# Kernel optimization log

Measured on AMD Instinct MI355X. Metric: run time of the kernel, lower is better.

The kernel has to match this reference:

```python
import jax, jax.numpy as jnp
import numpy as np

NUM_LAYERS = 32
IN_SIZE = 1024
OUT_SIZE = 1024
B, S = 32, 256


def setup_inputs() -> dict:
    key = jax.random.key(0)
    k1, k2, k3 = jax.random.split(key, 3)
    x = jax.random.normal(k1, (B, S, IN_SIZE), dtype=jnp.float32)
    layer_idx = jax.random.randint(k2, (S,), 0, NUM_LAYERS, dtype=jnp.int32)
    # learned parameter: per-layer weight [L, O, D], normal(stddev=1.0) as in flax init
    weight = jax.random.normal(k3, (NUM_LAYERS, OUT_SIZE, IN_SIZE), dtype=jnp.float32)
    return {"x": x, "layer_idx": layer_idx, "weight": weight}


def reference(x, layer_idx, weight):
    # x: [B, S, D]; layer_idx: [S]; weight: [L, O, D]
    # Each sequence position s uses expert weight[layer_idx[s]]:
    #   out[b, s, o] = sum_d x[b, s, d] * weight[layer_idx[s], o, d]
    w = weight[layer_idx]                      # [S, O, D] gather
    return jnp.einsum('bsd,sod->bso', x, w)    # [B, S, O]
```

## Files before the change

kernel.cpp:

```cpp
#include <hip/hip_runtime.h>
#include <hip/hip_bf16.h>
#include <stdint.h>

#define NLAYERS 32
#define DSIZE   1024
#define OSIZE   1024
#define BATCH   32
#define SEQ     256

#define WS_PERM  16
#define WS_TILE  512
#define MAX_TILES 88

typedef __attribute__((ext_vector_type(8)))  short short8;
typedef __attribute__((ext_vector_type(16))) float f32x16;

#define LDSTRIDE 72
#define BK 64
#define NSPLIT 16

__global__ void prep_kernel(const int* __restrict__ layer_idx, int* __restrict__ wsi) {
    __shared__ int cnt[NLAYERS];
    __shared__ int start_[NLAYERS];
    __shared__ int cursor[NLAYERS];
    const int t = threadIdx.x;
    if (t < NLAYERS) cnt[t] = 0;
    __syncthreads();
    int l = 0;
    if (t < SEQ) { l = layer_idx[t]; atomicAdd(&cnt[l], 1); }
    __syncthreads();
    if (t == 0) {
        int acc = 0;
        for (int i = 0; i < NLAYERS; ++i) { start_[i] = acc; cursor[i] = acc; acc += cnt[i]; }
    }
    __syncthreads();
    if (t < SEQ) {
        int r = atomicAdd(&cursor[l], 1);
        wsi[WS_PERM + r] = t;
    }
    if (t == 0) {
        int nt = 0;
        for (int i = 0; i < NLAYERS; ++i) {
            const int c = cnt[i];
            for (int j = 0; j < c; j += 4) {
                wsi[WS_TILE + nt*4 + 0] = i;
                wsi[WS_TILE + nt*4 + 1] = start_[i] + j;
                wsi[WS_TILE + nt*4 + 2] = (c - j < 4) ? (c - j) : 4;
                ++nt;
            }
        }
        wsi[0] = nt;
    }
}

static __device__ __forceinline__ unsigned pk2(float a, float b) {
    unsigned ua = __builtin_bit_cast(unsigned, a) + 0x8000u;
    unsigned ub = __builtin_bit_cast(unsigned, b) + 0x8000u;
    return __builtin_amdgcn_perm(ub, ua, 0x07060302u);
}

__global__ __launch_bounds__(256, 3) void gemm_kernel(
        const float* __restrict__ x, const float* __restrict__ wgt,
        const int* __restrict__ wsi, float* __restrict__ out) {
    const int ntiles = wsi[0];
    const int mt = blockIdx.y;
    if (mt >= ntiles) return;
    const int layer     = wsi[WS_TILE + mt*4 + 0];
    const int rank_base = wsi[WS_TILE + mt*4 + 1];
    const int nranks    = wsi[WS_TILE + mt*4 + 2];
    const int ntile     = blockIdx.x;

    __shared__ __align__(16) short ldsA[128 * LDSTRIDE];
    __shared__ __align__(16) short ldsB[64 * LDSTRIDE];

    const int t     = threadIdx.x;
    const int c4    = (t & 15) * 4;
    const int rbase = t >> 4;

    bool svalid[4];
    int  sv[4];
    #pragma unroll
    for (int j = 0; j < 4; ++j) {
        svalid[j] = (j < nranks);
        sv[j] = svalid[j] ? wsi[WS_PERM + rank_base + j] : 0;
    }

    const float* aptr[8];
    #pragma unroll
    for (int p = 0; p < 8; ++p) {
        const int roff = p >> 1;
        const int b    = rbase + ((p & 1) << 4);
        aptr[p] = x + (((size_t)(b * SEQ + sv[roff])) << 10) + c4;
    }
    const float* bbase = wgt + (((size_t)((layer << 10) + ntile * 64 + rbase)) << 10) + c4;

    float4 ra[8], rb[4];
    auto load_step = [&](int kk) {
        #pragma unroll
        for (int p = 0; p < 8; ++p) {
            if (svalid[p >> 1]) ra[p] = *(const float4*)(aptr[p] + kk);
            else                ra[p] = make_float4(0.f, 0.f, 0.f, 0.f);
        }
        #pragma unroll
        for (int p = 0; p < 4; ++p)
            rb[p] = *(const float4*)(bbase + ((size_t)p << 14) + kk);
    };

    const int lane = t & 63;
    const int wv   = t >> 6;
    const int wm   = wv * 32;
    const int l31  = lane & 31;
    const int lh   = lane >> 5;

    f32x16 acc[2];
    #pragma unroll
    for (int ni = 0; ni < 2; ++ni)
        #pragma unroll
        for (int r = 0; r < 16; ++r) acc[ni][r] = 0.f;

    const short* pA0 = &ldsA[(wm + l31) * LDSTRIDE + lh * 8];
    const short* pB0 = &ldsB[l31 * LDSTRIDE + lh * 8];

    load_step(0);
    #pragma unroll 1
    for (int kk = 0; kk < DSIZE; kk += BK) {
        __syncthreads();
        #pragma unroll
        for (int p = 0; p < 8; ++p) {
            const int row = rbase + 16 * p;
            uint2 va;
            va.x = pk2(ra[p].x, ra[p].y);
            va.y = pk2(ra[p].z, ra[p].w);
            *(uint2*)&ldsA[row * LDSTRIDE + c4] = va;
        }
        #pragma unroll
        for (int p = 0; p < 4; ++p) {
            const int row = rbase + 16 * p;
            uint2 vb;
            vb.x = pk2(rb[p].x, rb[p].y);
            vb.y = pk2(rb[p].z, rb[p].w);
            *(uint2*)&ldsB[row * LDSTRIDE + c4] = vb;
        }
        __syncthreads();
        if (kk + BK < DSIZE) load_step(kk + BK);
        #pragma unroll
        for (int sub = 0; sub < 4; ++sub) {
            short8 a0 = *(const short8*)(pA0 + sub*16);
            short8 b0 = *(const short8*)(pB0 + sub*16);
            short8 b1 = *(const short8*)(pB0 + 32*LDSTRIDE + sub*16);
            acc[0] = __builtin_amdgcn_mfma_f32_32x32x16_bf16(a0, b0, acc[0], 0, 0, 0);
            acc[1] = __builtin_amdgcn_mfma_f32_32x32x16_bf16(a0, b1, acc[1], 0, 0, 0);
        }
    }

    if (wv < nranks) {
        const int s = wsi[WS_PERM + rank_base + wv];
        #pragma unroll
        for (int ni = 0; ni < 2; ++ni) {
            const int ocol = ntile * 64 + ni * 32 + l31;
            #pragma unroll
            for (int r = 0; r < 16; ++r) {
                const int brow = (r & 3) + 8 * (r >> 2) + 4 * lh;
                out[(((size_t)(brow * SEQ + s)) << 10) + ocol] = acc[ni][r];
            }
        }
    }
}

extern "C" void kernel_launch(void* const* d_in, const int* in_sizes, int n_in,
                              void* d_out, int out_size, void* d_ws, size_t ws_size,
                              hipStream_t stream) {
    const float* x         = (const float*)d_in[0];
    const int*   layer_idx = (const int*)  d_in[1];
    const float* weight    = (const float*)d_in[2];
    float* out = (float*)d_out;
    int*   wsi = (int*)d_ws;

    prep_kernel<<<1, 256, 0, stream>>>(layer_idx, wsi);
    gemm_kernel<<<dim3(NSPLIT, MAX_TILES), 256, 0, stream>>>(x, weight, wsi, out);
}
```

Before: 251.4 us.

## Widen N tile to 128, split K in two with atomic accumulation

Each block now covers 128 output columns instead of 64, with four accumulators per wave, so every A tile loaded from global memory feeds twice as many MFMAs. The K dimension is split across two blocks via blockIdx.z, and partial results are combined with float atomicAdd into an output zeroed by hipMemsetAsync. BK drops to 32 and launch bounds rise to 4 blocks per SM. The cost is a memset pass over the output and atomic write traffic, and the summation order becomes nondeterministic.

```diff
diff --git a/kernel.cpp b/kernel.cpp
--- a/kernel.cpp
+++ b/kernel.cpp
@@ -15,9 +15,9 @@
 typedef __attribute__((ext_vector_type(8)))  short short8;
 typedef __attribute__((ext_vector_type(16))) float f32x16;
 
-#define LDSTRIDE 72
-#define BK 64
-#define NSPLIT 16
+#define LDSTRIDE 40
+#define BK 32
+#define KSPLIT 2
 
 __global__ void prep_kernel(const int* __restrict__ layer_idx, int* __restrict__ wsi) {
     __shared__ int cnt[NLAYERS];
@@ -59,7 +59,7 @@
     return __builtin_amdgcn_perm(ub, ua, 0x07060302u);
 }
 
-__global__ __launch_bounds__(256, 3) void gemm_kernel(
+__global__ __launch_bounds__(256, 4) void gemm_kernel(
         const float* __restrict__ x, const float* __restrict__ wgt,
         const int* __restrict__ wsi, float* __restrict__ out) {
     const int ntiles = wsi[0];
@@ -69,13 +69,14 @@
     const int rank_base = wsi[WS_TILE + mt*4 + 1];
     const int nranks    = wsi[WS_TILE + mt*4 + 2];
     const int ntile     = blockIdx.x;
+    const int koff      = blockIdx.z * (DSIZE / KSPLIT);
 
     __shared__ __align__(16) short ldsA[128 * LDSTRIDE];
-    __shared__ __align__(16) short ldsB[64 * LDSTRIDE];
+    __shared__ __align__(16) short ldsB[128 * LDSTRIDE];
 
     const int t     = threadIdx.x;
-    const int c4    = (t & 15) * 4;
-    const int rbase = t >> 4;
+    const int c4    = (t & 7) * 4;
+    const int rbase = t >> 3;
 
     bool svalid[4];
     int  sv[4];
@@ -85,25 +86,22 @@
         sv[j] = svalid[j] ? wsi[WS_PERM + rank_base + j] : 0;
     }
 
-    const float* aptr[8];
+    const float* aptr[4];
     #pragma unroll
-    for (int p = 0; p < 8; ++p) {
-        const int roff = p >> 1;
-        const int b    = rbase + ((p & 1) << 4);
-        aptr[p] = x + (((size_t)(b * SEQ + sv[roff])) << 10) + c4;
-    }
-    const float* bbase = wgt + (((size_t)((layer << 10) + ntile * 64 + rbase)) << 10) + c4;
+    for (int p = 0; p < 4; ++p)
+        aptr[p] = x + (((size_t)(rbase * SEQ + sv[p])) << 10) + koff + c4;
+    const float* bbase = wgt + (((size_t)((layer << 10) + ntile * 128 + rbase)) << 10) + koff + c4;
 
-    float4 ra[8], rb[4];
+    float4 ra[4], rb[4];
     auto load_step = [&](int kk) {
         #pragma unroll
-        for (int p = 0; p < 8; ++p) {
-            if (svalid[p >> 1]) ra[p] = *(const float4*)(aptr[p] + kk);
-            else                ra[p] = make_float4(0.f, 0.f, 0.f, 0.f);
+        for (int p = 0; p < 4; ++p) {
+            if (svalid[p]) ra[p] = *(const float4*)(aptr[p] + kk);
+            else           ra[p] = make_float4(0.f, 0.f, 0.f, 0.f);
         }
         #pragma unroll
         for (int p = 0; p < 4; ++p)
-            rb[p] = *(const float4*)(bbase + ((size_t)p << 14) + kk);
+            rb[p] = *(const float4*)(bbase + ((size_t)(32 * p) << 10) + kk);
     };
 
     const int lane = t & 63;
@@ -112,9 +110,9 @@
     const int l31  = lane & 31;
     const int lh   = lane >> 5;
 
-    f32x16 acc[2];
+    f32x16 acc[4];
     #pragma unroll
-    for (int ni = 0; ni < 2; ++ni)
+    for (int ni = 0; ni < 4; ++ni)
         #pragma unroll
         for (int r = 0; r < 16; ++r) acc[ni][r] = 0.f;
 
@@ -123,11 +121,11 @@
 
     load_step(0);
     #pragma unroll 1
-    for (int kk = 0; kk < DSIZE; kk += BK) {
+    for (int kk = 0; kk < DSIZE / KSPLIT; kk += BK) {
         __syncthreads();
         #pragma unroll
-        for (int p = 0; p < 8; ++p) {
-            const int row = rbase + 16 * p;
+        for (int p = 0; p < 4; ++p) {
+            const int row = rbase + 32 * p;
             uint2 va;
             va.x = pk2(ra[p].x, ra[p].y);
             va.y = pk2(ra[p].z, ra[p].w);
@@ -135,33 +133,34 @@
         }
         #pragma unroll
         for (int p = 0; p < 4; ++p) {
-            const int row = rbase + 16 * p;
+            const int row = rbase + 32 * p;
             uint2 vb;
             vb.x = pk2(rb[p].x, rb[p].y);
             vb.y = pk2(rb[p].z, rb[p].w);
             *(uint2*)&ldsB[row * LDSTRIDE + c4] = vb;
         }
         __syncthreads();
-        if (kk + BK < DSIZE) load_step(kk + BK);
+        if (kk + BK < DSIZE / KSPLIT) load_step(kk + BK);
         #pragma unroll
-        for (int sub = 0; sub < 4; ++sub) {
+        for (int sub = 0; sub < 2; ++sub) {
             short8 a0 = *(const short8*)(pA0 + sub*16);
-            short8 b0 = *(const short8*)(pB0 + sub*16);
-            short8 b1 = *(const short8*)(pB0 + 32*LDSTRIDE + sub*16);
-            acc[0] = __builtin_amdgcn_mfma_f32_32x32x16_bf16(a0, b0, acc[0], 0, 0, 0);
-            acc[1] = __builtin_amdgcn_mfma_f32_32x32x16_bf16(a0, b1, acc[1], 0, 0, 0);
+            #pragma unroll
+            for (int ni = 0; ni < 4; ++ni) {
+                short8 b = *(const short8*)(pB0 + 32*ni*LDSTRIDE + sub*16);
+                acc[ni] = __builtin_amdgcn_mfma_f32_32x32x16_bf16(a0, b, acc[ni], 0, 0, 0);
+            }
         }
     }
 
     if (wv < nranks) {
-        const int s = wsi[WS_PERM + rank_base + wv];
+        const int s = sv[wv];
         #pragma unroll
-        for (int ni = 0; ni < 2; ++ni) {
-            const int ocol = ntile * 64 + ni * 32 + l31;
+        for (int ni = 0; ni < 4; ++ni) {
+            const int ocol = ntile * 128 + ni * 32 + l31;
             #pragma unroll
             for (int r = 0; r < 16; ++r) {
                 const int brow = (r & 3) + 8 * (r >> 2) + 4 * lh;
-                out[(((size_t)(brow * SEQ + s)) << 10) + ocol] = acc[ni][r];
+                atomicAdd(&out[(((size_t)(brow * SEQ + s)) << 10) + ocol], acc[ni][r]);
             }
         }
     }
@@ -176,6 +175,7 @@
     float* out = (float*)d_out;
     int*   wsi = (int*)d_ws;
 
+    hipMemsetAsync(out, 0, (size_t)out_size * sizeof(float), stream);
     prep_kernel<<<1, 256, 0, stream>>>(layer_idx, wsi);
-    gemm_kernel<<<dim3(NSPLIT, MAX_TILES), 256, 0, stream>>>(x, weight, wsi, out);
+    gemm_kernel<<<dim3(8, MAX_TILES, KSPLIT), 256, 0, stream>>>(x, weight, wsi, out);
 }
```

New measurement: 284.2 us. 13.0% more time.
